# Kernel tuning notes

Measured on AMD Instinct MI355X. Metric: run time of the kernel, lower is better.

Reference implementation:

```python
import jax, jax.numpy as jnp
from jax import lax
import numpy as np

CHI, CHO = 256, 256
B, H, W = 4, 64, 64
KH = KW = 3
K = KH * KW
EPS = 1e-5


def setup_inputs() -> dict:
    key = jax.random.key(0)
    ks = jax.random.split(key, 8)
    x = jax.random.normal(ks[0], (B, CHI, H, W), jnp.float32)
    # offset/mask conv: chi -> 3*K channels (dy[K], dx[K], mask[K]); small init so offsets stay local
    w_off = jax.random.normal(ks[1], (3 * K, CHI, KH, KW), jnp.float32) * 0.01
    b_off = jax.random.normal(ks[2], (3 * K,), jnp.float32) * 0.01
    weight = jax.random.normal(ks[3], (CHO, CHI, KH, KW), jnp.float32) * 0.05
    bias = jax.random.normal(ks[4], (CHO,), jnp.float32) * 0.05
    gamma = 1.0 + 0.1 * jax.random.normal(ks[5], (CHO,), jnp.float32)
    beta = 0.1 * jax.random.normal(ks[6], (CHO,), jnp.float32)
    rmean = 0.1 * jax.random.normal(ks[7], (CHO,), jnp.float32)
    rvar = jnp.ones((CHO,), jnp.float32)
    return {"x": x, "w_off": w_off, "b_off": b_off, "weight": weight,
            "bias": bias, "gamma": gamma, "beta": beta, "rmean": rmean, "rvar": rvar}


def _dcn_bn_relu(x, w_off, b_off, weight, bias, gamma, beta, rmean, rvar):
    Bn, C, Hn, Wn = x.shape
    cho = weight.shape[0]
    # offset/mask branch: ordinary 3x3 same conv
    om = lax.conv_general_dilated(x, w_off, (1, 1), ((1, 1), (1, 1)),
                                  dimension_numbers=("NCHW", "OIHW", "NCHW"))
    om = om + b_off[None, :, None, None]
    o1, o2, m = jnp.split(om, 3, axis=1)            # each [B,K,H,W]
    mask = jax.nn.sigmoid(m).transpose(0, 2, 3, 1)  # [B,H,W,K]
    dy = o1.transpose(0, 2, 3, 1)                   # [B,H,W,K]
    dx = o2.transpose(0, 2, 3, 1)
    # sampling coords: p = out_pos - pad + k*dil + offset (stride=1, pad=1, dil=1)
    ky = jnp.repeat(jnp.arange(KH, dtype=x.dtype) - 1.0, KW)  # [K]
    kx = jnp.tile(jnp.arange(KW, dtype=x.dtype) - 1.0, KH)
    py = jnp.arange(Hn, dtype=x.dtype)[None, :, None, None] + ky + dy  # [B,H,W,K]
    px = jnp.arange(Wn, dtype=x.dtype)[None, None, :, None] + kx + dx

    xt = x.transpose(0, 2, 3, 1)  # [B,H,W,C]
    y0 = jnp.floor(py)
    x0 = jnp.floor(px)
    ly = py - y0
    lx = px - x0
    y0i = y0.astype(jnp.int32)
    x0i = x0.astype(jnp.int32)

    def corner(yi, xi, w):
        valid = (yi >= 0) & (yi < Hn) & (xi >= 0) & (xi < Wn)
        yc = jnp.clip(yi, 0, Hn - 1)
        xc = jnp.clip(xi, 0, Wn - 1)
        v = jax.vmap(lambda img, a, b: img[a, b])(xt, yc, xc)  # [B,H,W,K,C]
        return v * (w * valid.astype(x.dtype))[..., None]

    val = (corner(y0i, x0i, (1 - ly) * (1 - lx))
           + corner(y0i, x0i + 1, (1 - ly) * lx)
           + corner(y0i + 1, x0i, ly * (1 - lx))
           + corner(y0i + 1, x0i + 1, ly * lx))  # [B,H,W,K,C]

    cols = val * mask[..., None]  # modulated columns [B,H,W,K,C]
    wk = weight.reshape(cho, weight.shape[1], K)  # [O,C,K]
    out = jnp.einsum("bhwkc,ock->bohw", cols, wk) + bias[None, :, None, None]
    # BatchNorm (eval: running stats) + ReLU
    inv = gamma * lax.rsqrt(rvar + EPS)
    out = out * inv[None, :, None, None] + (beta - rmean * inv)[None, :, None, None]
    return jax.nn.relu(out)


def reference(x, w_off, b_off, weight, bias, gamma, beta, rmean, rvar):
    return _dcn_bn_relu(x, w_off, b_off, weight, bias, gamma, beta, rmean, rvar)
```

## Files before the change

### kernel.cpp

```cpp
#include <hip/hip_runtime.h>
#include <math.h>

#define NH 64
#define NW 64
#define NB 4
#define CHI 256
#define CHO 256
#define XT_B (66 * 66 * 256)

typedef __attribute__((ext_vector_type(8))) short bf16x8;
typedef __attribute__((ext_vector_type(4))) float f32x4;

static __device__ __forceinline__ unsigned short f2bf(float f) {
    unsigned int u = __float_as_uint(f);
    u += 0x7fffu + ((u >> 16) & 1u);
    return (unsigned short)(u >> 16);
}
static __device__ __forceinline__ float bflo(unsigned int p) { return __uint_as_float(p << 16); }
static __device__ __forceinline__ float bfhi(unsigned int p) { return __uint_as_float(p & 0xffff0000u); }
static __device__ __forceinline__ unsigned int pkbf(float a, float b) {
    unsigned int r;
    asm("v_cvt_pk_bf16_f32 %0, %1, %2" : "=v"(r) : "v"(a), "v"(b));
    return r;
}

#define BAR_LGKM() asm volatile("s_waitcnt lgkmcnt(0)\n\ts_barrier" ::: "memory")


__global__ __launch_bounds__(256) void prep_all(const float* __restrict__ weight,
                                                const float* __restrict__ w_off,
                                                const float* __restrict__ x,
                                                unsigned short* __restrict__ wB,
                                                unsigned short* __restrict__ wOB,
                                                unsigned short* __restrict__ xT) {
    __shared__ unsigned short sT[64 * 134];
    int bid = blockIdx.x, tid = threadIdx.x;
    if (bid < 2304) {
        int idx = bid * 256 + tid;
        int kin = idx & 31, o = (idx >> 5) & 255, ks = idx >> 13;
        int cc = ks / 9, kt = ks - cc * 9;
        int c = cc * 32 + kin;
        wB[idx] = f2bf(weight[((size_t)o * CHI + c) * 9 + kt]);
    } else if (bid < 2592) {
        int idx = (bid - 2304) * 256 + tid;
        int kin = idx & 31, oc = (idx >> 5) & 31, ks = idx >> 10;
        int cc = ks / 9, kt = ks - cc * 9;
        int c = cc * 32 + kin;
        wOB[idx] = (oc < 27) ? f2bf(w_off[((size_t)oc * CHI + c) * 9 + kt])
                             : (unsigned short)0;
    } else if (bid < 3104) {
        int bid2 = bid - 2592;
        int b = bid2 >> 7, rem = bid2 & 127;
        int y = rem >> 1, chalf = rem & 1;
        int c0 = chalf * 128;
        for (int rep = 0; rep < 8; ++rep) {
            int idx = rep * 256 + tid;
            int c = idx >> 4, p4 = (idx & 15) * 4;
            const float* src = x + (((size_t)b * CHI + c0 + c) * 64 + y) * 64 + p4;
            float4 v = *(const float4*)src;
            sT[(p4 + 0) * 134 + c] = f2bf(v.x);
            sT[(p4 + 1) * 134 + c] = f2bf(v.y);
            sT[(p4 + 2) * 134 + c] = f2bf(v.z);
            sT[(p4 + 3) * 134 + c] = f2bf(v.w);
        }
        __syncthreads();
        unsigned int* dst = (unsigned int*)(xT + ((size_t)(b * 66 + y + 1) * 66 + 1) * 256)
                          + chalf * 64;
        for (int rep = 0; rep < 16; ++rep) {
            int idx = rep * 256 + tid;
            int px = idx >> 6, cu = idx & 63;
            unsigned int lo = sT[px * 134 + cu * 2];
            unsigned int hi = sT[px * 134 + cu * 2 + 1];
            dst[(size_t)px * 128 + cu] = lo | (hi << 16);
        }
    } else {
        int flat = (bid - 3104) * 256 + tid;
        int b = flat / 33280, r = flat - b * 33280;
        unsigned int* xtu = (unsigned int*)xT;
        size_t base = (size_t)b * 66 * 66 * 128;
        size_t idx;
        if (r < 8448) {
            idx = base + r;
        } else if (r < 16896) {
            idx = base + (size_t)65 * 66 * 128 + (r - 8448);
        } else {
            int rc = r - 16896;
            int side = rc >> 13;
            int row = 1 + ((rc & 8191) >> 7);
            int cu = rc & 127;
            idx = base + ((size_t)row * 66 + (side ? 65 : 0)) * 128 + cu;
        }
        xtu[idx] = 0;
    }
}

__global__ __launch_bounds__(512) void dcn_fused(
        const unsigned short* __restrict__ xT,
        const unsigned short* __restrict__ wOB,
        const unsigned short* __restrict__ wB,
        const float* __restrict__ b_off,
        const float* __restrict__ bias, const float* __restrict__ gamma,
        const float* __restrict__ beta, const float* __restrict__ rmean,
        const float* __restrict__ rvar, float* __restrict__ out) {
    __shared__ __align__(16) unsigned char smem[33280];
    int4*   s_po = (int4*)smem;
    float4* s_cw = (float4*)(smem + 4608);
    unsigned short* sA = (unsigned short*)(smem + 9216);
    float* sOff = (float*)(smem + 9216);
    float (*sOut)[260] = (float(*)[260])smem;

    int id = blockIdx.x;
    int xcd = id & 7, sl = id >> 3;
    int b = xcd >> 1;
    int h = (xcd & 1) * 32 + (sl & 31);
    int pxbase = (sl >> 5) * 32;

    int tid = threadIdx.x;
    int lane = tid & 63, q = tid >> 6;
    int ln = lane & 15, lk = lane >> 4;
    int nb = q & 3, kh = q >> 2;

    const unsigned short* xTfull = xT + (size_t)b * XT_B;
    const bf16x8* wOBv = (const bf16x8*)wOB;
    const bf16x8* wBv  = (const bf16x8*)wB;

    {
        int omt = q & 1, ont = (q >> 1) & 1, okq = q >> 2;
        int opx = pxbase + omt * 16 + ln;
        int oposbase = (h + 1) * 66 + opx + 1;
        f32x4 oacc = {0.f, 0.f, 0.f, 0.f};
        for (int s = okq * 36; s < okq * 36 + 36; ++s) {
            int cc = s / 9, kt = s - cc * 9;
            int pos = oposbase + (kt / 3 - 1) * 66 + (kt % 3 - 1);
            bf16x8 af  = *(const bf16x8*)&xTfull[(size_t)pos * 256 + cc * 32 + lk * 8];
            bf16x8 bfo = wOBv[((size_t)s * 32 + ont * 16 + ln) * 4 + lk];
            oacc = __builtin_amdgcn_mfma_f32_16x16x32_bf16(af, bfo, oacc, 0, 0, 0);
        }
#pragma unroll
        for (int r = 0; r < 4; ++r)
            sOff[(okq * 32 + omt * 16 + lk * 4 + r) * 33 + ont * 16 + ln] = oacc[r];
    }
    BAR_LGKM();

    for (int p = tid; p < 288; p += 512) {
        int k = p >> 5, pwl = p & 31, pw = pxbase + pwl;
        float dy = sOff[pwl * 33 + k]        + sOff[(32 + pwl) * 33 + k]        + b_off[k];
        float dx = sOff[pwl * 33 + k + 9]    + sOff[(32 + pwl) * 33 + k + 9]    + b_off[k + 9];
        float mp = sOff[pwl * 33 + k + 18]   + sOff[(32 + pwl) * 33 + k + 18]   + b_off[k + 18];
        float mv = 1.f / (1.f + __expf(-mp));
        float py  = (float)h  + (float)(k / 3 - 1) + dy;
        float pxf = (float)pw + (float)(k % 3 - 1) + dx;
        float y0f = floorf(py), x0f = floorf(pxf);
        int y0 = (int)y0f, x0 = (int)x0f;
        float ly = py - y0f, lx = pxf - x0f;
        int y0c = min(max(y0, -1), 64), y1c = min(max(y0 + 1, -1), 64);
        int x0c = min(max(x0, -1), 64), x1c = min(max(x0 + 1, -1), 64);
        int ry0 = (y0c + 1) * 66, ry1 = (y1c + 1) * 66;
        s_po[p] = make_int4(ry0 + x0c + 1, ry0 + x1c + 1, ry1 + x0c + 1, ry1 + x1c + 1);
        s_cw[p] = make_float4((1.f - ly) * (1.f - lx) * mv, (1.f - ly) * lx * mv,
                              ly * (1.f - lx) * mv,         ly * lx * mv);
    }

    int cg8 = tid & 3, pxl = (tid >> 2) & 31, sl4 = tid >> 7;
    int khp = sl4 >> 1, ip = sl4 & 1;
    const unsigned short* xTb = xTfull + cg8 * 8;

    f32x4 zf = {0.f, 0.f, 0.f, 0.f};
    f32x4 acc[2][4] = {{zf, zf, zf, zf}, {zf, zf, zf, zf}};

    uint4 C00, C01, C10, C11;

#define LOADS(s) do { int s_ = (s); int cc_ = s_ / 9; int kt_ = s_ - cc_ * 9;  \
        int4 o4_ = s_po[kt_ * 32 + pxl];                                       \
        const unsigned short* cb_ = xTb + cc_ * 32;                            \
        C00 = *(const uint4*)(cb_ + (size_t)o4_.x * 256);                      \
        C01 = *(const uint4*)(cb_ + (size_t)o4_.y * 256);                      \
        C10 = *(const uint4*)(cb_ + (size_t)o4_.z * 256);                      \
        C11 = *(const uint4*)(cb_ + (size_t)o4_.w * 256);                      \
    } while (0)

#define WRITEA(s, buf) do { int s_ = (s); int kt_ = s_ - (s_ / 9) * 9;         \
        float4 w_ = s_cw[kt_ * 32 + pxl];                                      \
        uint4 pk_;                                                             \
        pk_.x = pkbf(w_.x*bflo(C00.x)+w_.y*bflo(C01.x)+w_.z*bflo(C10.x)+w_.w*bflo(C11.x), \
                     w_.x*bfhi(C00.x)+w_.y*bfhi(C01.x)+w_.z*bfhi(C10.x)+w_.w*bfhi(C11.x)); \
        pk_.y = pkbf(w_.x*bflo(C00.y)+w_.y*bflo(C01.y)+w_.z*bflo(C10.y)+w_.w*bflo(C11.y), \
                     w_.x*bfhi(C00.y)+w_.y*bfhi(C01.y)+w_.z*bfhi(C10.y)+w_.w*bfhi(C11.y)); \
        pk_.z = pkbf(w_.x*bflo(C00.z)+w_.y*bflo(C01.z)+w_.z*bflo(C10.z)+w_.w*bflo(C11.z), \
                     w_.x*bfhi(C00.z)+w_.y*bfhi(C01.z)+w_.z*bfhi(C10.z)+w_.w*bfhi(C11.z)); \
        pk_.w = pkbf(w_.x*bflo(C00.w)+w_.y*bflo(C01.w)+w_.z*bflo(C10.w)+w_.w*bflo(C11.w), \
                     w_.x*bfhi(C00.w)+w_.y*bfhi(C01.w)+w_.z*bfhi(C10.w)+w_.w*bfhi(C11.w)); \
        *(uint4*)&sA[(buf) * 1280 + pxl * 40 + cg8 * 8] = pk_;                 \
    } while (0)

    BAR_LGKM();

    LOADS(khp * 36 + ip);
    WRITEA(khp * 36 + ip, sl4);
    LOADS(khp * 36 + 2 + ip);
    bf16x8 bf[4], nbf[4];
#pragma unroll
    for (int j = 0; j < 4; ++j)
        bf[j] = wBv[((size_t)(kh * 36) * 256 + nb * 64 + j * 16 + ln) * 4 + lk];
    BAR_LGKM();

    for (int g = 0; g < 18; ++g) {
        if (g + 1 < 18) WRITEA(khp * 36 + 2 * (g + 1) + ip, ((g + 1) & 1) * 4 + sl4);
        if (g + 2 < 18) LOADS(khp * 36 + 2 * (g + 2) + ip);
#pragma unroll
        for (int i = 0; i < 2; ++i) {
            int off = 2 * g + i;
            int buf = (g & 1) * 4 + kh * 2 + i;
            bf16x8 af0 = *(const bf16x8*)&sA[buf * 1280 + ln * 40 + lk * 8];
            bf16x8 af1 = *(const bf16x8*)&sA[buf * 1280 + (16 + ln) * 40 + lk * 8];
            bool more = (off + 1 < 36);
            if (more) {
                int sn = kh * 36 + off + 1;
#pragma unroll
                for (int j = 0; j < 4; ++j)
                    nbf[j] = wBv[((size_t)sn * 256 + nb * 64 + j * 16 + ln) * 4 + lk];
            }
#pragma unroll
            for (int j = 0; j < 4; ++j) {
                acc[0][j] = __builtin_amdgcn_mfma_f32_16x16x32_bf16(af0, bf[j], acc[0][j], 0, 0, 0);
                acc[1][j] = __builtin_amdgcn_mfma_f32_16x16x32_bf16(af1, bf[j], acc[1][j], 0, 0, 0);
            }
            if (more) {
#pragma unroll
                for (int j = 0; j < 4; ++j) bf[j] = nbf[j];
            }
        }
        BAR_LGKM();
    }
#undef LOADS
#undef WRITEA

    if (kh == 1) {
#pragma unroll
        for (int m = 0; m < 2; ++m)
#pragma unroll
            for (int j = 0; j < 4; ++j) {
                int oc = nb * 64 + j * 16 + ln;
#pragma unroll
                for (int r = 0; r < 4; ++r)
                    sOut[m * 16 + lk * 4 + r][oc] = acc[m][j][r];
            }
    }
    __syncthreads();
    if (kh == 0) {
#pragma unroll
        for (int m = 0; m < 2; ++m)
#pragma unroll
            for (int j = 0; j < 4; ++j) {
                int oc = nb * 64 + j * 16 + ln;
                float inv = gamma[oc] * rsqrtf(rvar[oc] + 1e-5f);
                float sh  = beta[oc] - rmean[oc] * inv + bias[oc] * inv;
                int row = m * 16 + lk * 4;
                float4 rr;
                rr.x = fmaxf((acc[m][j][0] + sOut[row + 0][oc]) * inv + sh, 0.f);
                rr.y = fmaxf((acc[m][j][1] + sOut[row + 1][oc]) * inv + sh, 0.f);
                rr.z = fmaxf((acc[m][j][2] + sOut[row + 2][oc]) * inv + sh, 0.f);
                rr.w = fmaxf((acc[m][j][3] + sOut[row + 3][oc]) * inv + sh, 0.f);
                size_t oi = (((size_t)b * 256 + oc) * 64 + h) * 64 + pxbase + row;
                *(float4*)(out + oi) = rr;
            }
    }
}

extern "C" void kernel_launch(void* const* d_in, const int* in_sizes, int n_in,
                              void* d_out, int out_size, void* d_ws, size_t ws_size,
                              hipStream_t stream) {
    const float* x      = (const float*)d_in[0];
    const float* w_off  = (const float*)d_in[1];
    const float* b_off  = (const float*)d_in[2];
    const float* weight = (const float*)d_in[3];
    const float* bias   = (const float*)d_in[4];
    const float* gamma  = (const float*)d_in[5];
    const float* beta   = (const float*)d_in[6];
    const float* rmean  = (const float*)d_in[7];
    const float* rvar   = (const float*)d_in[8];
    float* out = (float*)d_out;

    unsigned short* wB  = (unsigned short*)d_ws;
    unsigned short* wOB = wB + 589824;
    unsigned short* xT  = wOB + 73728;

    hipLaunchKernelGGL(prep_all, dim3(3624), dim3(256), 0, stream,
                       weight, w_off, x, wB, wOB, xT);
    hipLaunchKernelGGL(dcn_fused, dim3(512), dim3(512), 0, stream,
                       xT, wOB, wB, b_off, bias, gamma, beta, rmean, rvar, out);
}
```

Baseline: 156.3 us.

## Split offset-conv accumulators, double-buffer weight fragments, and set occupancy launch bound

The offset conv loop is unrolled over the 9 taps and alternates between two accumulators, which breaks the serial MFMA dependency chain. The main loop now keeps two weight fragment sets (even and odd k-steps) and refills each right after it is used, which removes the register copy and gives each global load more time to arrive. A min-blocks hint of 4 is added to __launch_bounds__, and the epilogue hoists the BN parameter loads out of the m loop. The launch-bound hint may force register spilling, and the extra fragment set raises register pressure.

Measured after the change: 155.9 us. Within noise of the previous version (-0.3%).

```diff
diff --git a/kernel.cpp b/kernel.cpp
--- a/kernel.cpp
+++ b/kernel.cpp
@@ -94,7 +94,7 @@
     }
 }
 
-__global__ __launch_bounds__(512) void dcn_fused(
+__global__ __launch_bounds__(512, 4) void dcn_fused(
         const unsigned short* __restrict__ xT,
         const unsigned short* __restrict__ wOB,
         const unsigned short* __restrict__ wB,
@@ -128,17 +128,20 @@
         int omt = q & 1, ont = (q >> 1) & 1, okq = q >> 2;
         int opx = pxbase + omt * 16 + ln;
         int oposbase = (h + 1) * 66 + opx + 1;
-        f32x4 oacc = {0.f, 0.f, 0.f, 0.f};
-        for (int s = okq * 36; s < okq * 36 + 36; ++s) {
-            int cc = s / 9, kt = s - cc * 9;
-            int pos = oposbase + (kt / 3 - 1) * 66 + (kt % 3 - 1);
-            bf16x8 af  = *(const bf16x8*)&xTfull[(size_t)pos * 256 + cc * 32 + lk * 8];
-            bf16x8 bfo = wOBv[((size_t)s * 32 + ont * 16 + ln) * 4 + lk];
-            oacc = __builtin_amdgcn_mfma_f32_16x16x32_bf16(af, bfo, oacc, 0, 0, 0);
+        f32x4 oa0 = {0.f, 0.f, 0.f, 0.f}, oa1 = {0.f, 0.f, 0.f, 0.f};
+        for (int cc = okq * 4; cc < okq * 4 + 4; ++cc) {
+#pragma unroll
+            for (int kt = 0; kt < 9; ++kt) {
+                int pos = oposbase + (kt / 3 - 1) * 66 + (kt % 3 - 1);
+                bf16x8 af = *(const bf16x8*)&xTfull[(size_t)pos * 256 + cc * 32 + lk * 8];
+                bf16x8 bo = wOBv[((size_t)(cc * 9 + kt) * 32 + ont * 16 + ln) * 4 + lk];
+                if (kt & 1) oa1 = __builtin_amdgcn_mfma_f32_16x16x32_bf16(af, bo, oa1, 0, 0, 0);
+                else        oa0 = __builtin_amdgcn_mfma_f32_16x16x32_bf16(af, bo, oa0, 0, 0, 0);
+            }
         }
 #pragma unroll
         for (int r = 0; r < 4; ++r)
-            sOff[(okq * 32 + omt * 16 + lk * 4 + r) * 33 + ont * 16 + ln] = oacc[r];
+            sOff[(okq * 32 + omt * 16 + lk * 4 + r) * 33 + ont * 16 + ln] = oa0[r] + oa1[r];
     }
     BAR_LGKM();
 
@@ -198,37 +201,45 @@
     LOADS(khp * 36 + ip);
     WRITEA(khp * 36 + ip, sl4);
     LOADS(khp * 36 + 2 + ip);
-    bf16x8 bf[4], nbf[4];
-#pragma unroll
-    for (int j = 0; j < 4; ++j)
-        bf[j] = wBv[((size_t)(kh * 36) * 256 + nb * 64 + j * 16 + ln) * 4 + lk];
+    bf16x8 bfE[4], bfO[4];
+#pragma unroll
+    for (int j = 0; j < 4; ++j) {
+        bfE[j] = wBv[((size_t)(kh * 36 + 0) * 256 + nb * 64 + j * 16 + ln) * 4 + lk];
+        bfO[j] = wBv[((size_t)(kh * 36 + 1) * 256 + nb * 64 + j * 16 + ln) * 4 + lk];
+    }
     BAR_LGKM();
 
     for (int g = 0; g < 18; ++g) {
         if (g + 1 < 18) WRITEA(khp * 36 + 2 * (g + 1) + ip, ((g + 1) & 1) * 4 + sl4);
         if (g + 2 < 18) LOADS(khp * 36 + 2 * (g + 2) + ip);
-#pragma unroll
-        for (int i = 0; i < 2; ++i) {
-            int off = 2 * g + i;
-            int buf = (g & 1) * 4 + kh * 2 + i;
-            bf16x8 af0 = *(const bf16x8*)&sA[buf * 1280 + ln * 40 + lk * 8];
-            bf16x8 af1 = *(const bf16x8*)&sA[buf * 1280 + (16 + ln) * 40 + lk * 8];
-            bool more = (off + 1 < 36);
-            if (more) {
-                int sn = kh * 36 + off + 1;
-#pragma unroll
-                for (int j = 0; j < 4; ++j)
-                    nbf[j] = wBv[((size_t)sn * 256 + nb * 64 + j * 16 + ln) * 4 + lk];
-            }
-#pragma unroll
-            for (int j = 0; j < 4; ++j) {
-                acc[0][j] = __builtin_amdgcn_mfma_f32_16x16x32_bf16(af0, bf[j], acc[0][j], 0, 0, 0);
-                acc[1][j] = __builtin_amdgcn_mfma_f32_16x16x32_bf16(af1, bf[j], acc[1][j], 0, 0, 0);
-            }
-            if (more) {
-#pragma unroll
-                for (int j = 0; j < 4; ++j) bf[j] = nbf[j];
-            }
+
+        int bufb = (g & 1) * 4 + kh * 2;
+        const unsigned short* pA0 = &sA[bufb * 1280];
+        const unsigned short* pA1 = &sA[bufb * 1280 + 1280];
+        bf16x8 a00 = *(const bf16x8*)&pA0[ln * 40 + lk * 8];
+        bf16x8 a01 = *(const bf16x8*)&pA0[(16 + ln) * 40 + lk * 8];
+        bf16x8 a10 = *(const bf16x8*)&pA1[ln * 40 + lk * 8];
+        bf16x8 a11 = *(const bf16x8*)&pA1[(16 + ln) * 40 + lk * 8];
+
+#pragma unroll
+        for (int j = 0; j < 4; ++j) {
+            acc[0][j] = __builtin_amdgcn_mfma_f32_16x16x32_bf16(a00, bfE[j], acc[0][j], 0, 0, 0);
+            acc[1][j] = __builtin_amdgcn_mfma_f32_16x16x32_bf16(a01, bfE[j], acc[1][j], 0, 0, 0);
+        }
+        if (2 * g + 2 < 36) {
+#pragma unroll
+            for (int j = 0; j < 4; ++j)
+                bfE[j] = wBv[((size_t)(kh * 36 + 2 * g + 2) * 256 + nb * 64 + j * 16 + ln) * 4 + lk];
+        }
+#pragma unroll
+        for (int j = 0; j < 4; ++j) {
+            acc[0][j] = __builtin_amdgcn_mfma_f32_16x16x32_bf16(a10, bfO[j], acc[0][j], 0, 0, 0);
+            acc[1][j] = __builtin_amdgcn_mfma_f32_16x16x32_bf16(a11, bfO[j], acc[1][j], 0, 0, 0);
+        }
+        if (2 * g + 3 < 36) {
+#pragma unroll
+            for (int j = 0; j < 4; ++j)
+                bfO[j] = wBv[((size_t)(kh * 36 + 2 * g + 3) * 256 + nb * 64 + j * 16 + ln) * 4 + lk];
         }
         BAR_LGKM();
     }
@@ -249,12 +260,12 @@
     __syncthreads();
     if (kh == 0) {
 #pragma unroll
-        for (int m = 0; m < 2; ++m)
-#pragma unroll
-            for (int j = 0; j < 4; ++j) {
-                int oc = nb * 64 + j * 16 + ln;
-                float inv = gamma[oc] * rsqrtf(rvar[oc] + 1e-5f);
-                float sh  = beta[oc] - rmean[oc] * inv + bias[oc] * inv;
+        for (int j = 0; j < 4; ++j) {
+            int oc = nb * 64 + j * 16 + ln;
+            float inv = gamma[oc] * rsqrtf(rvar[oc] + 1e-5f);
+            float sh  = beta[oc] - rmean[oc] * inv + bias[oc] * inv;
+#pragma unroll
+            for (int m = 0; m < 2; ++m) {
                 int row = m * 16 + lk * 4;
                 float4 rr;
                 rr.x = fmaxf((acc[m][j][0] + sOut[row + 0][oc]) * inv + sh, 0.f);
@@ -264,6 +275,7 @@
                 size_t oi = (((size_t)b * 256 + oc) * 64 + h) * 64 + pxbase + row;
                 *(float4*)(out + oi) = rr;
             }
+        }
     }
 }
 
```
